# Optimization experiments

Hardware: AMD Instinct MI355X
Metric: run time of the kernel (lower is better)

Reference implementation:

```python
import jax, jax.numpy as jnp
import numpy as np

D_MODEL, D_STATE, D_CONV, EXPAND, D_EXPERT = 768, 16, 4, 2, 4
D_INNER = EXPAND * D_MODEL            # 1536
N_EXP = D_STATE // D_EXPERT           # 4 state experts
DT_RANK = -(-D_MODEL // 16)           # 48
B, L = 4, 512


def setup_inputs() -> dict:
    key = jax.random.key(0)
    ks = jax.random.split(key, 16)
    f = lambda k, shape, s=0.02: jax.random.normal(k, shape, dtype=jnp.float32) * s
    # dt bias init: inverse-softplus of dt ~ LogUniform[1e-3, 1e-1] (as in __init__)
    dt = jnp.exp(jax.random.uniform(ks[13], (D_INNER,)) * (np.log(0.1) - np.log(0.001)) + np.log(0.001))
    inv_dt = dt + jnp.log(-jnp.expm1(-dt))
    # A_log = log(arange(1..d_state)) broadcast to (d_inner, d_state)
    A_log = jnp.log(jnp.broadcast_to(jnp.arange(1, D_STATE + 1, dtype=jnp.float32), (D_INNER, D_STATE)))
    return {
        "hidden_states": jax.random.normal(ks[0], (B, L, D_MODEL), dtype=jnp.float32),
        "in_proj_w": f(ks[1], (2 * D_INNER, D_MODEL)),
        "conv_w": f(ks[2], (D_INNER, 1, D_CONV), 0.25),
        "conv_b": jnp.zeros(D_INNER, jnp.float32),
        "conv_w_b": f(ks[3], (D_INNER, 1, D_CONV), 0.25),
        "conv_b_b": jnp.zeros(D_INNER, jnp.float32),
        "x_proj_w": f(ks[4], (DT_RANK + 2 * D_STATE, D_INNER)),
        "x_proj_w_bwd": f(ks[5], (DT_RANK + 2 * D_STATE, D_INNER)),
        "dt_proj_w": f(ks[6], (D_INNER, DT_RANK), DT_RANK ** -0.5),
        "dt_proj_bias": inv_dt,
        "dt_proj_w_bwd": f(ks[7], (D_INNER, DT_RANK), DT_RANK ** -0.5),
        "dt_proj_bias_bwd": inv_dt,
        "A_log": A_log,
        "A_b_log": A_log,
        "D": jnp.ones(D_INNER, jnp.float32),
        "D_b": jnp.ones(D_INNER, jnp.float32),
        "mlp_w1": f(ks[8], (D_INNER, D_INNER)),
        "mlp_b1": jnp.zeros(D_INNER, jnp.float32),
        "mlp_w2": f(ks[9], (N_EXP, D_INNER)),
        "mlp_b2": jnp.zeros(N_EXP, jnp.float32),
        "out_proj_w": f(ks[10], (D_MODEL, D_INNER)),
    }


def _causal_conv_silu(x, w, b):
    # x: (B, D_INNER, L); depthwise causal conv, kernel D_CONV, left pad D_CONV-1
    y = jax.lax.conv_general_dilated(
        x, w, window_strides=(1,), padding=[(D_CONV - 1, 0)],
        dimension_numbers=("NCH", "OIH", "NCH"), feature_group_count=D_INNER)
    return jax.nn.silu(y + b[None, :, None])


def _selective_scan_experts(xc, Wx, Wdt, bdt, A_log):
    # xc: (B, D_INNER, L) post-conv activations. Returns per-expert outputs
    # (B, L, D_INNER, N_EXP) and xc transposed (B, L, D_INNER).
    xt = jnp.swapaxes(xc, 1, 2)                              # (B, L, D)
    x_dbl = jnp.einsum("bld,ed->ble", xt, Wx)               # (B, L, R+2N)
    dtr, Bm, Cm = jnp.split(x_dbl, [DT_RANK, DT_RANK + D_STATE], axis=-1)
    delta = jax.nn.softplus(jnp.einsum("blr,dr->bld", dtr, Wdt) + bdt)  # (B,L,D)
    A = -jnp.exp(A_log)                                      # (D, N), negative
    dA = jnp.exp(delta[..., None] * A)                       # (B,L,D,N)
    dBx = delta[..., None] * Bm[:, :, None, :] * xt[..., None]

    def step(h, inp):
        dA_t, dBx_t = inp
        h = dA_t * h + dBx_t
        return h, h

    h0 = jnp.zeros((xt.shape[0], D_INNER, D_STATE), xt.dtype)
    _, hs = jax.lax.scan(step, h0, (jnp.moveaxis(dA, 1, 0), jnp.moveaxis(dBx, 1, 0)))
    hs = jnp.moveaxis(hs, 0, 1)                              # (B,L,D,N)
    # partition d_state into N_EXP experts of D_EXPERT states; contract C per expert
    hs_e = hs.reshape(hs.shape[0], hs.shape[1], D_INNER, N_EXP, D_EXPERT)
    C_e = Cm.reshape(Cm.shape[0], Cm.shape[1], N_EXP, D_EXPERT)
    y_e = jnp.einsum("bldek,blek->blde", hs_e, C_e)          # (B,L,D,E)
    return y_e, xt


def reference(hidden_states, in_proj_w, conv_w, conv_b, conv_w_b, conv_b_b,
              x_proj_w, x_proj_w_bwd, dt_proj_w, dt_proj_bias, dt_proj_w_bwd,
              dt_proj_bias_bwd, A_log, A_b_log, D, D_b, mlp_w1, mlp_b1,
              mlp_w2, mlp_b2, out_proj_w):
    xz = jnp.einsum("bld,ed->bel", hidden_states, in_proj_w)  # (B, 2*D_INNER, L)
    x, z = jnp.split(xz, 2, axis=1)
    xb, zb = jnp.split(xz[..., ::-1], 2, axis=1)              # flipped sequence
    xc = _causal_conv_silu(x, conv_w, conv_b)
    xcb = _causal_conv_silu(xb, conv_w_b, conv_b_b)
    y_e, xt = _selective_scan_experts(xc, x_proj_w, dt_proj_w, dt_proj_bias, A_log)
    yb_e, xbt = _selective_scan_experts(xcb, x_proj_w_bwd, dt_proj_w_bwd, dt_proj_bias_bwd, A_b_log)
    # router: MLP(silu) -> sigmoid, then softmax over experts (as in torch forward)
    h1 = jax.nn.silu(jnp.einsum("bld,hd->blh", xt, mlp_w1) + mlp_b1)
    gate = jax.nn.sigmoid(jnp.einsum("blh,eh->ble", h1, mlp_w2) + mlp_b2)
    w = jax.nn.softmax(gate, axis=-1)                         # (B,L,E)
    zt, zbt = jnp.swapaxes(z, 1, 2), jnp.swapaxes(zb, 1, 2)
    # gated expert mixture + skip (D) term, then z-gate (silu), per direction.
    # Note: same forward-order router weights applied to the flipped-direction
    # outputs before the final flip, matching the torch code exactly.
    y = (jnp.einsum("blde,ble->bld", y_e, w) + xt * D) * jax.nn.silu(zt)
    yb = (jnp.einsum("blde,ble->bld", yb_e, w) + xbt * D_b) * jax.nn.silu(zbt)
    yb = yb[:, ::-1, :]                                       # flip back to forward order
    return jnp.einsum("bld,od->blo", y + yb, out_proj_w)
```

## Files before the change

### kernel.cpp

```cpp
#include <hip/hip_runtime.h>
#include <math.h>

#define ACT_NONE 0
#define ACT_SILU 1
#define ACT_SOFTPLUS 2

constexpr int kDModel = 768;
constexpr int kDInner = 1536;
constexpr int kDtRank = 48;
constexpr int kB = 4;
constexpr int kL = 512;
constexpr int kTok = kB * kL;
constexpr int kCH = 32;
constexpr int kNCH = kL / kCH;
constexpr int kSumStride = kDInner * 16;
constexpr int kXSplit = 6;
constexpr int kXKchunk = kDInner / kXSplit;

typedef __attribute__((ext_vector_type(8))) short short8v;
typedef __attribute__((ext_vector_type(8))) unsigned short ushort8v;
typedef __attribute__((ext_vector_type(4))) float f32x4;

__device__ __forceinline__ float act_apply_f(float x, int act) {
    if (act == ACT_SILU) return x / (1.f + __expf(-x));
    if (act == ACT_SOFTPLUS) return (x > 20.f) ? x : log1pf(__expf(x));
    return x;
}

__device__ __forceinline__ unsigned short f2bf(float f) {
    unsigned u = __float_as_uint(f);
    u += 0x7fff + ((u >> 16) & 1);
    return (unsigned short)(u >> 16);
}
__device__ __forceinline__ float bf2f(unsigned short h) {
    return __uint_as_float((unsigned)h << 16);
}
__device__ __forceinline__ ushort8v addbf8(ushort8v a, ushort8v b) {
    ushort8v r;
    #pragma unroll
    for (int i = 0; i < 8; ++i)
        r[i] = f2bf(bf2f(a[i]) + bf2f(b[i]));
    return r;
}

__device__ __forceinline__ void xcd_swz(int& bx, int& by, int& bz) {
    int gX = gridDim.x, gY = gridDim.y;
    int nwg = gX * gY * gridDim.z;
    int lin = bx + gX * (by + gY * bz);
    int chunk = nwg >> 3;
    int lin2 = (lin & 7) * chunk + (lin >> 3);
    bx = lin2 % gX;
    int t = lin2 / gX;
    by = t % gY;
    bz = t / gY;
}

template<int ACT, int HASBIAS, int DUAL, int SPLITK>
__global__ __launch_bounds__(256, 3)
void gemm_bf16(const unsigned short* __restrict__ A16,
               const unsigned short* __restrict__ A2,
               const unsigned short* __restrict__ W16,
               const float* __restrict__ bias,
               float* __restrict__ C,
               int M, int N, int K)
{
    __shared__ unsigned short Al[2][64][40];
    __shared__ unsigned short Bl[2][128][40];
    int bx = blockIdx.x, by = blockIdx.y, bz = blockIdx.z;
    xcd_swz(bx, by, bz);
    const int tid = threadIdx.x;
    const int row0 = by * 64;
    const int col0 = bx * 128;
    const int kc = K / SPLITK;
    const int k0base = bz * kc;

    const int srowA = tid >> 2;
    const int skA   = (tid & 3) << 3;
    const int srowB = tid >> 1;
    const int skB   = (tid & 1) << 4;

    const int w = tid >> 6;
    const int lane = tid & 63;
    const int wr = (w & 1) * 32;
    const int wc = (w >> 1) * 64;
    const int fr = lane & 15;
    const int fk = (lane >> 4) * 8;

    f32x4 acc[2][4] = {};

    const unsigned short* aptr = A16 + (size_t)(row0 + srowA) * K + k0base + skA;
    const unsigned short* aptr2 = DUAL ? (A2 + (size_t)(row0 + srowA) * K + k0base + skA) : nullptr;
    const unsigned short* bptr = W16 + (size_t)(col0 + srowB) * K + k0base + skB;

    ushort8v ra, rb0, rb1;
    auto gload = [&](int k0) {
        ra = *(const ushort8v*)(aptr + k0);
        if (DUAL) {
            ushort8v c0 = *(const ushort8v*)(aptr2 + k0);
            ra = addbf8(ra, c0);
        }
        rb0 = *(const ushort8v*)(bptr + k0);
        rb1 = *(const ushort8v*)(bptr + k0 + 8);
    };
    auto swrite = [&](int buf) {
        *(ushort8v*)&Al[buf][srowA][skA]     = ra;
        *(ushort8v*)&Bl[buf][srowB][skB]     = rb0;
        *(ushort8v*)&Bl[buf][srowB][skB + 8] = rb1;
    };

    gload(0);
    swrite(0);
    __syncthreads();

    const int nsteps = kc >> 5;
    for (int s = 0; s < nsteps; ++s) {
        const int cur = s & 1;
        if (s + 1 < nsteps) gload((s + 1) << 5);
        short8v afrag[2], bfrag[4];
        #pragma unroll
        for (int i = 0; i < 2; ++i)
            afrag[i] = *(const short8v*)&Al[cur][wr + i * 16 + fr][fk];
        #pragma unroll
        for (int j = 0; j < 4; ++j)
            bfrag[j] = *(const short8v*)&Bl[cur][wc + j * 16 + fr][fk];
        #pragma unroll
        for (int i = 0; i < 2; ++i)
            #pragma unroll
            for (int j = 0; j < 4; ++j)
                acc[i][j] = __builtin_amdgcn_mfma_f32_16x16x32_bf16(
                    afrag[i], bfrag[j], acc[i][j], 0, 0, 0);
        if (s + 1 < nsteps) swrite(cur ^ 1);
        __syncthreads();
    }

    const int orow = (lane >> 4) * 4;
    #pragma unroll
    for (int i = 0; i < 2; ++i) {
        #pragma unroll
        for (int j = 0; j < 4; ++j) {
            const int ccol = col0 + wc + j * 16 + fr;
            float bv = HASBIAS ? bias[ccol] : 0.f;
            #pragma unroll
            for (int r = 0; r < 4; ++r) {
                const int crow = row0 + wr + i * 16 + orow + r;
                float v = acc[i][j][r];
                if (SPLITK > 1) {
                    C[(size_t)bz * M * N + (size_t)crow * N + ccol] = v;
                } else {
                    v += bv;
                    C[(size_t)crow * N + ccol] = act_apply_f(v, ACT);
                }
            }
        }
    }
}

__global__ __launch_bounds__(256)
void reduce_out(const float* __restrict__ part, float* __restrict__ out, int n4)
{
    int i = blockIdx.x * 256 + threadIdx.x;
    if (i >= n4) return;
    float4 a = ((const float4*)part)[i];
    float4 b = ((const float4*)(part))[i + n4];
    float4 o;
    o.x = a.x + b.x; o.y = a.y + b.y; o.z = a.z + b.z; o.w = a.w + b.w;
    ((float4*)out)[i] = o;
}

__global__ __launch_bounds__(256, 2)
void xproj_mfma(const unsigned short* __restrict__ ahi_f, const unsigned short* __restrict__ alo_f,
                const unsigned short* __restrict__ ahi_b, const unsigned short* __restrict__ alo_b,
                const unsigned short* __restrict__ wxhi,
                const unsigned short* __restrict__ wxlo,
                float* __restrict__ xpart)
{
    __shared__ unsigned short Ah[128][40], Av[128][40], Bh[128][40], Bv[128][40];
    const int tid = threadIdx.x;
    const int row0 = blockIdx.x * 128;
    const int dir = blockIdx.y;
    const int split = blockIdx.z;
    const int ks = split * kXKchunk;

    const unsigned short* ahi = dir ? ahi_b : ahi_f;
    const unsigned short* alo = dir ? alo_b : alo_f;
    const unsigned short* whi = wxhi + (size_t)dir * 128 * kDInner;
    const unsigned short* wlo = wxlo + (size_t)dir * 128 * kDInner;

    const int srow = tid >> 1;
    const int sk   = (tid & 1) << 4;
    const int w = tid >> 6;
    const int lane = tid & 63;
    const int wr = (w >> 1) * 64;
    const int wc = (w & 1) * 64;
    const int fr = lane & 15;
    const int fk = (lane >> 4) * 8;

    f32x4 acc[4][4] = {};

    const unsigned short* pah = ahi + (size_t)(row0 + srow) * kDInner + ks + sk;
    const unsigned short* pal = alo + (size_t)(row0 + srow) * kDInner + ks + sk;
    const unsigned short* pbh = whi + (size_t)srow * kDInner + ks + sk;
    const unsigned short* pbl = wlo + (size_t)srow * kDInner + ks + sk;

    ushort8v rah0, rah1, ral0, ral1, rbh0, rbh1, rbl0, rbl1;
    auto gload = [&](int k0) {
        rah0 = *(const ushort8v*)(pah + k0); rah1 = *(const ushort8v*)(pah + k0 + 8);
        ral0 = *(const ushort8v*)(pal + k0); ral1 = *(const ushort8v*)(pal + k0 + 8);
        rbh0 = *(const ushort8v*)(pbh + k0); rbh1 = *(const ushort8v*)(pbh + k0 + 8);
        rbl0 = *(const ushort8v*)(pbl + k0); rbl1 = *(const ushort8v*)(pbl + k0 + 8);
    };
    auto swrite = [&]() {
        *(ushort8v*)&Ah[srow][sk] = rah0; *(ushort8v*)&Ah[srow][sk + 8] = rah1;
        *(ushort8v*)&Av[srow][sk] = ral0; *(ushort8v*)&Av[srow][sk + 8] = ral1;
        *(ushort8v*)&Bh[srow][sk] = rbh0; *(ushort8v*)&Bh[srow][sk + 8] = rbh1;
        *(ushort8v*)&Bv[srow][sk] = rbl0; *(ushort8v*)&Bv[srow][sk + 8] = rbl1;
    };

    gload(0);
    const int nsteps = kXKchunk >> 5;
    for (int s = 0; s < nsteps; ++s) {
        swrite();
        __syncthreads();
        if (s + 1 < nsteps) gload((s + 1) << 5);
        short8v ah[4], al[4], bh[4], bl[4];
        #pragma unroll
        for (int i = 0; i < 4; ++i) {
            ah[i] = *(const short8v*)&Ah[wr + i * 16 + fr][fk];
            al[i] = *(const short8v*)&Av[wr + i * 16 + fr][fk];
            bh[i] = *(const short8v*)&Bh[wc + i * 16 + fr][fk];
            bl[i] = *(const short8v*)&Bv[wc + i * 16 + fr][fk];
        }
        #pragma unroll
        for (int i = 0; i < 4; ++i)
            #pragma unroll
            for (int j = 0; j < 4; ++j) {
                acc[i][j] = __builtin_amdgcn_mfma_f32_16x16x32_bf16(ah[i], bh[j], acc[i][j], 0, 0, 0);
                acc[i][j] = __builtin_amdgcn_mfma_f32_16x16x32_bf16(ah[i], bl[j], acc[i][j], 0, 0, 0);
                acc[i][j] = __builtin_amdgcn_mfma_f32_16x16x32_bf16(al[i], bh[j], acc[i][j], 0, 0, 0);
            }
        __syncthreads();
    }

    float* outp = xpart + (size_t)(dir * kXSplit + split) * kTok * 80;
    const int orow = (lane >> 4) * 4;
    #pragma unroll
    for (int i = 0; i < 4; ++i)
        #pragma unroll
        for (int j = 0; j < 4; ++j) {
            const int ccol = wc + j * 16 + fr;
            if (ccol < 80) {
                #pragma unroll
                for (int r = 0; r < 4; ++r) {
                    const int crow = row0 + wr + i * 16 + orow + r;
                    outp[(size_t)crow * 80 + ccol] = acc[i][j][r];
                }
            }
        }
}

__global__ __launch_bounds__(256)
void xproj_reduce(const float* __restrict__ xpart,
                  float* __restrict__ xdbl_f, float* __restrict__ xdbl_b,
                  unsigned short* __restrict__ dtr_hi,
                  unsigned short* __restrict__ dtr_lo)
{
    int i = blockIdx.x * 256 + threadIdx.x;
    const int per = kTok * 96;
    int dir = i >= per;
    int rem = dir ? i - per : i;
    int t = rem / 96;
    int c = rem - t * 96;
    const int plane = kTok * 80;
    if (c < 80) {
        const float* base = xpart + (size_t)dir * kXSplit * plane;
        float s = 0.f;
        #pragma unroll
        for (int k = 0; k < kXSplit; ++k) s += base[(size_t)k * plane + t * 80 + c];
        (dir ? xdbl_b : xdbl_f)[(size_t)t * 80 + c] = s;
        if (c < kDtRank) {
            size_t o = ((size_t)dir * kTok + t) * 64 + c;
            unsigned short h = f2bf(s);
            dtr_hi[o] = h;
            dtr_lo[o] = f2bf(s - bf2f(h));
        }
    } else {
        int pc = c - 80 + kDtRank;
        size_t o = ((size_t)dir * kTok + t) * 64 + pc;
        dtr_hi[o] = 0;
        dtr_lo[o] = 0;
    }
}

__global__ __launch_bounds__(256, 2)
void dtproj_mfma(const unsigned short* __restrict__ dtr_hi, const unsigned short* __restrict__ dtr_lo,
                 const unsigned short* __restrict__ wdt_hi, const unsigned short* __restrict__ wdt_lo,
                 const float* __restrict__ bias_f, const float* __restrict__ bias_b,
                 float* __restrict__ delta_f, float* __restrict__ delta_b)
{
    __shared__ unsigned short Ah[128][40], Av[128][40], Bh[128][40], Bv[128][40];
    const int tid = threadIdx.x;
    const int col0 = blockIdx.x * 128;
    const int row0 = blockIdx.y * 128;
    const int dir = blockIdx.z;

    const unsigned short* ahi = dtr_hi + (size_t)dir * kTok * 64;
    const unsigned short* alo = dtr_lo + (size_t)dir * kTok * 64;
    const unsigned short* bhi = wdt_hi + (size_t)dir * kDInner * 64;
    const unsigned short* blo = wdt_lo + (size_t)dir * kDInner * 64;
    const float* bias = dir ? bias_b : bias_f;
    float* delta = dir ? delta_b : delta_f;

    const int srow = tid >> 1;
    const int sk   = (tid & 1) << 4;
    const int w = tid >> 6;
    const int lane = tid & 63;
    const int wr = (w >> 1) * 64;
    const int wc = (w & 1) * 64;
    const int fr = lane & 15;
    const int fk = (lane >> 4) * 8;

    f32x4 acc[4][4] = {};

    const unsigned short* pah = ahi + (size_t)(row0 + srow) * 64 + sk;
    const unsigned short* pal = alo + (size_t)(row0 + srow) * 64 + sk;
    const unsigned short* pbh = bhi + (size_t)(col0 + srow) * 64 + sk;
    const unsigned short* pbl = blo + (size_t)(col0 + srow) * 64 + sk;

    ushort8v rah0, rah1, ral0, ral1, rbh0, rbh1, rbl0, rbl1;
    auto gload = [&](int k0) {
        rah0 = *(const ushort8v*)(pah + k0); rah1 = *(const ushort8v*)(pah + k0 + 8);
        ral0 = *(const ushort8v*)(pal + k0); ral1 = *(const ushort8v*)(pal + k0 + 8);
        rbh0 = *(const ushort8v*)(pbh + k0); rbh1 = *(const ushort8v*)(pbh + k0 + 8);
        rbl0 = *(const ushort8v*)(pbl + k0); rbl1 = *(const ushort8v*)(pbl + k0 + 8);
    };
    auto swrite = [&]() {
        *(ushort8v*)&Ah[srow][sk] = rah0; *(ushort8v*)&Ah[srow][sk + 8] = rah1;
        *(ushort8v*)&Av[srow][sk] = ral0; *(ushort8v*)&Av[srow][sk + 8] = ral1;
        *(ushort8v*)&Bh[srow][sk] = rbh0; *(ushort8v*)&Bh[srow][sk + 8] = rbh1;
        *(ushort8v*)&Bv[srow][sk] = rbl0; *(ushort8v*)&Bv[srow][sk + 8] = rbl1;
    };

    gload(0);
    #pragma unroll
    for (int s = 0; s < 2; ++s) {
        swrite();
        __syncthreads();
        if (s == 0) gload(32);
        short8v ah[4], al[4], bh[4], bl[4];
        #pragma unroll
        for (int i = 0; i < 4; ++i) {
            ah[i] = *(const short8v*)&Ah[wr + i * 16 + fr][fk];
            al[i] = *(const short8v*)&Av[wr + i * 16 + fr][fk];
            bh[i] = *(const short8v*)&Bh[wc + i * 16 + fr][fk];
            bl[i] = *(const short8v*)&Bv[wc + i * 16 + fr][fk];
        }
        #pragma unroll
        for (int i = 0; i < 4; ++i)
            #pragma unroll
            for (int j = 0; j < 4; ++j) {
                acc[i][j] = __builtin_amdgcn_mfma_f32_16x16x32_bf16(ah[i], bh[j], acc[i][j], 0, 0, 0);
                acc[i][j] = __builtin_amdgcn_mfma_f32_16x16x32_bf16(ah[i], bl[j], acc[i][j], 0, 0, 0);
                acc[i][j] = __builtin_amdgcn_mfma_f32_16x16x32_bf16(al[i], bh[j], acc[i][j], 0, 0, 0);
            }
        __syncthreads();
    }

    const int orow = (lane >> 4) * 4;
    #pragma unroll
    for (int i = 0; i < 4; ++i)
        #pragma unroll
        for (int j = 0; j < 4; ++j) {
            const int ccol = col0 + wc + j * 16 + fr;
            const float bv = bias[ccol];
            #pragma unroll
            for (int r = 0; r < 4; ++r) {
                const int crow = row0 + wr + i * 16 + orow + r;
                float x = acc[i][j][r] + bv;
                delta[(size_t)crow * kDInner + ccol] = (x > 20.f) ? x : log1pf(__expf(x));
            }
        }
}

__global__ __launch_bounds__(256)
void convert4_kernel(const float* __restrict__ s0, unsigned short* __restrict__ d0, int n0,
                     const float* __restrict__ s1, unsigned short* __restrict__ d1, int n1,
                     const float* __restrict__ s2, unsigned short* __restrict__ d2, int n2,
                     const float* __restrict__ s3, unsigned short* __restrict__ d3, int n3)
{
    int i = blockIdx.x * 256 + threadIdx.x;
    const float* s; unsigned short* d; int loc;
    if (i < n0) { s = s0; d = d0; loc = i; }
    else if (i < n0 + n1) { s = s1; d = d1; loc = i - n0; }
    else if (i < n0 + n1 + n2) { s = s2; d = d2; loc = i - n0 - n1; }
    else if (i < n0 + n1 + n2 + n3) { s = s3; d = d3; loc = i - n0 - n1 - n2; }
    else return;
    float4 v = ((const float4*)s)[loc];
    ushort4 o;
    o.x = f2bf(v.x); o.y = f2bf(v.y); o.z = f2bf(v.z); o.w = f2bf(v.w);
    ((ushort4*)d)[loc] = o;
}

__global__ __launch_bounds__(256)
void convert_w_kernel(const float* __restrict__ Wxf, const float* __restrict__ Wxb,
                      const float* __restrict__ Wdtf, const float* __restrict__ Wdtb,
                      unsigned short* __restrict__ wxhi, unsigned short* __restrict__ wxlo,
                      unsigned short* __restrict__ wdthi, unsigned short* __restrict__ wdtlo)
{
    int i = blockIdx.x * 256 + threadIdx.x;
    const int nx = 2 * 128 * kDInner / 4;
    const int ndt_per = kDInner * 16;
    if (i < nx) {
        const int per_dir = 128 * kDInner / 4;
        int dir = i >= per_dir;
        int rem = dir ? i - per_dir : i;
        int r = rem / (kDInner / 4);
        int k4 = rem - r * (kDInner / 4);
        ushort4 oh = {0, 0, 0, 0}, ol = {0, 0, 0, 0};
        if (r < 80) {
            const float* W = dir ? Wxb : Wxf;
            float4 v = ((const float4*)W)[r * (kDInner / 4) + k4];
            oh.x = f2bf(v.x); ol.x = f2bf(v.x - bf2f(oh.x));
            oh.y = f2bf(v.y); ol.y = f2bf(v.y - bf2f(oh.y));
            oh.z = f2bf(v.z); ol.z = f2bf(v.z - bf2f(oh.z));
            oh.w = f2bf(v.w); ol.w = f2bf(v.w - bf2f(oh.w));
        }
        size_t o = ((size_t)dir * 128 + r) * kDInner + k4 * 4;
        *(ushort4*)(wxhi + o) = oh;
        *(ushort4*)(wxlo + o) = ol;
    } else {
        int j = i - nx;
        if (j >= 2 * ndt_per) return;
        int dir = j >= ndt_per;
        int rem = dir ? j - ndt_per : j;
        int r = rem >> 4;
        int k4 = rem & 15;
        ushort4 oh = {0, 0, 0, 0}, ol = {0, 0, 0, 0};
        if (k4 < 12) {
            const float* W = dir ? Wdtb : Wdtf;
            float4 v = ((const float4*)W)[r * 12 + k4];
            oh.x = f2bf(v.x); ol.x = f2bf(v.x - bf2f(oh.x));
            oh.y = f2bf(v.y); ol.y = f2bf(v.y - bf2f(oh.y));
            oh.z = f2bf(v.z); ol.z = f2bf(v.z - bf2f(oh.z));
            oh.w = f2bf(v.w); ol.w = f2bf(v.w - bf2f(oh.w));
        }
        size_t o = ((size_t)dir * kDInner + r) * 64 + k4 * 4;
        *(ushort4*)(wdthi + o) = oh;
        *(ushort4*)(wdtlo + o) = ol;
    }
}

__global__ __launch_bounds__(256)
void conv_both_kernel(const float* __restrict__ xz,
                      const float* __restrict__ w_f, const float* __restrict__ b_f,
                      const float* __restrict__ w_b, const float* __restrict__ b_b,
                      unsigned short* __restrict__ hi_f, unsigned short* __restrict__ hi_b,
                      unsigned short* __restrict__ lo_f, unsigned short* __restrict__ lo_b)
{
    __shared__ float s_x[131][64];
    const int tid = threadIdx.x;
    const int d0 = blockIdx.x * 64;
    const int b = blockIdx.y;
    const int dir = blockIdx.z;

    const float* w    = dir ? w_b : w_f;
    const float* bias = dir ? b_b : b_f;
    unsigned short* hi = dir ? hi_b : hi_f;
    unsigned short* lo = dir ? lo_b : lo_f;

    const int cd = tid & 63;
    const int lp = tid >> 6;
    float4 wv = *(const float4*)(w + (size_t)(d0 + cd) * 4);
    float bsv = bias[d0 + cd];

    for (int ch = 0; ch < 4; ++ch) {
        const int lbase = ch * 128;
        if (tid < 192) {
            int h = tid >> 6, dl = tid & 63;
            int l = lbase - 3 + h;
            float v = 0.f;
            if (l >= 0) {
                int ls = dir ? (kL - 1 - l) : l;
                v = xz[((size_t)(b * kL + ls)) * 3072 + d0 + dl];
            }
            s_x[h][dl] = v;
        }
        #pragma unroll
        for (int k = 0; k < 32; ++k) {
            int idx = k * 256 + tid;
            int li = idx >> 6, dl = idx & 63;
            int l = lbase + li;
            int ls = dir ? (kL - 1 - l) : l;
            s_x[3 + li][dl] = xz[((size_t)(b * kL + ls)) * 3072 + d0 + dl];
        }
        __syncthreads();
        #pragma unroll 4
        for (int i = 0; i < 32; ++i) {
            int li = lp * 32 + i;
            float acc = bsv;
            acc = fmaf(s_x[li + 0][cd], wv.x, acc);
            acc = fmaf(s_x[li + 1][cd], wv.y, acc);
            acc = fmaf(s_x[li + 2][cd], wv.z, acc);
            acc = fmaf(s_x[li + 3][cd], wv.w, acc);
            float o = acc / (1.f + __expf(-acc));
            size_t oi = ((size_t)(b * kL + lbase + li)) * kDInner + d0 + cd;
            unsigned short h = f2bf(o);
            hi[oi] = h;
            lo[oi] = f2bf(o - bf2f(h));
        }
        __syncthreads();
    }
}

__global__ __launch_bounds__(256)
void gate_kernel(const float* __restrict__ h1,
                 const float* __restrict__ w2,
                 const float* __restrict__ b2,
                 float* __restrict__ wgt)
{
    int wave = threadIdx.x >> 6;
    int lane = threadIdx.x & 63;
    int t = blockIdx.x * 4 + wave;
    const float* hrow = h1 + (size_t)t * kDInner;
    float acc[4] = {0.f, 0.f, 0.f, 0.f};
    for (int h = lane; h < kDInner; h += 64) {
        float hv = hrow[h];
        #pragma unroll
        for (int e = 0; e < 4; ++e)
            acc[e] = fmaf(hv, w2[e * kDInner + h], acc[e]);
    }
    #pragma unroll
    for (int e = 0; e < 4; ++e) {
        #pragma unroll
        for (int off = 32; off > 0; off >>= 1)
            acc[e] += __shfl_xor(acc[e], off);
    }
    if (lane == 0) {
        float g[4], m = -1e30f, s = 0.f;
        #pragma unroll
        for (int e = 0; e < 4; ++e) {
            g[e] = 1.f / (1.f + __expf(-(acc[e] + b2[e])));
            m = fmaxf(m, g[e]);
        }
        #pragma unroll
        for (int e = 0; e < 4; ++e) { g[e] = __expf(g[e] - m); s += g[e]; }
        float inv = 1.f / s;
        #pragma unroll
        for (int e = 0; e < 4; ++e) wgt[(size_t)t * 4 + e] = g[e] * inv;
    }
}

__global__ __launch_bounds__(256)
void scan_sum_kernel(const float* __restrict__ delta_f, const float* __restrict__ delta_b,
                     const unsigned short* __restrict__ xhi_f, const unsigned short* __restrict__ xlo_f,
                     const unsigned short* __restrict__ xhi_b, const unsigned short* __restrict__ xlo_b,
                     const float* __restrict__ xdbl_f, const float* __restrict__ xdbl_b,
                     const float* __restrict__ A_log, const float* __restrict__ A_b_log,
                     float* __restrict__ Aprod, float* __restrict__ hfin)
{
    __shared__ float s_dlt[kCH][64];
    __shared__ float s_x[kCH][64];
    __shared__ float s_b[kCH][16];

    const int tid = threadIdx.x;
    const int d0 = blockIdx.x * 64;
    const int c = blockIdx.y;
    const int z = blockIdx.z;
    const int b = z >> 1;
    const int dir = z & 1;

    const float* delta = dir ? delta_b : delta_f;
    const unsigned short* xhi = dir ? xhi_b : xhi_f;
    const unsigned short* xlo = dir ? xlo_b : xlo_f;
    const float* xdbl  = dir ? xdbl_b : xdbl_f;
    const float* Alog  = dir ? A_b_log : A_log;

    const int l0 = c * kCH;
    #pragma unroll
    for (int k = 0; k < 2; ++k) {
        int idx = k * 256 + tid;
        int l = idx >> 4, d4 = (idx & 15) << 2;
        size_t t = (size_t)(b * kL + l0 + l);
        float4 dv = *(const float4*)(delta + t * kDInner + d0 + d4);
        *(float4*)&s_dlt[l][d4] = dv;
        ushort4 hv = *(const ushort4*)(xhi + t * kDInner + d0 + d4);
        ushort4 lv = *(const ushort4*)(xlo + t * kDInner + d0 + d4);
        float4 xv;
        xv.x = bf2f(hv.x) + bf2f(lv.x); xv.y = bf2f(hv.y) + bf2f(lv.y);
        xv.z = bf2f(hv.z) + bf2f(lv.z); xv.w = bf2f(hv.w) + bf2f(lv.w);
        *(float4*)&s_x[l][d4] = xv;
    }
    if (tid < 128) {
        int l = tid >> 2, c4 = (tid & 3) << 2;
        *(float4*)&s_b[l][c4] =
            *(const float4*)(xdbl + ((size_t)(b * kL + l0 + l)) * 80 + kDtRank + c4);
    }
    const int e = tid & 3;
    const int dd = tid >> 2;
    const int d = d0 + dd;
    float An[4];
    #pragma unroll
    for (int u = 0; u < 4; ++u)
        An[u] = -__expf(Alog[(size_t)d * 16 + e * 4 + u]);
    __syncthreads();

    float h[4] = {0.f, 0.f, 0.f, 0.f};
    float sdlt = 0.f;
    const int e4 = e * 4;
    #pragma unroll 8
    for (int li = 0; li < kCH; ++li) {
        float dlt = s_dlt[li][dd];
        float xv  = s_x[li][dd];
        float dx = dlt * xv;
        sdlt += dlt;
        float4 Bv = *(const float4*)&s_b[li][e4];
        h[0] = fmaf(__expf(dlt * An[0]), h[0], dx * Bv.x);
        h[1] = fmaf(__expf(dlt * An[1]), h[1], dx * Bv.y);
        h[2] = fmaf(__expf(dlt * An[2]), h[2], dx * Bv.z);
        h[3] = fmaf(__expf(dlt * An[3]), h[3], dx * Bv.w);
    }
    size_t base = ((size_t)z * kNCH + c) * kSumStride + (size_t)d * 16 + e4;
    float4 ap, hf;
    ap.x = __expf(An[0] * sdlt); ap.y = __expf(An[1] * sdlt);
    ap.z = __expf(An[2] * sdlt); ap.w = __expf(An[3] * sdlt);
    hf.x = h[0]; hf.y = h[1]; hf.z = h[2]; hf.w = h[3];
    *(float4*)(Aprod + base) = ap;
    *(float4*)(hfin + base)  = hf;
}

__global__ __launch_bounds__(256)
void scan_comb_kernel(float* __restrict__ Aprod, const float* __restrict__ hfin)
{
    int g = blockIdx.x * 256 + threadIdx.x;
    int z = g / kSumStride;
    int rem = g - z * kSumStride;
    float h = 0.f;
    #pragma unroll
    for (int c = 0; c < kNCH; ++c) {
        size_t idx = ((size_t)z * kNCH + c) * kSumStride + rem;
        float A  = Aprod[idx];
        float hf = hfin[idx];
        Aprod[idx] = h;
        h = fmaf(A, h, hf);
    }
}

__global__ __launch_bounds__(256)
void scan_fix_kernel(const float* __restrict__ delta_f, const float* __restrict__ delta_b,
                     const unsigned short* __restrict__ xhi_f, const unsigned short* __restrict__ xlo_f,
                     const unsigned short* __restrict__ xhi_b, const unsigned short* __restrict__ xlo_b,
                     const float* __restrict__ xdbl_f, const float* __restrict__ xdbl_b,
                     const float* __restrict__ A_log, const float* __restrict__ A_b_log,
                     const float* __restrict__ Dp, const float* __restrict__ D_b,
                     const float* __restrict__ wgt, const float* __restrict__ xz,
                     const float* __restrict__ hin,
                     unsigned short* __restrict__ y16_f, unsigned short* __restrict__ y16_b)
{
    __shared__ float s_dlt[kCH][64];
    __shared__ float s_x[kCH][64];
    __shared__ float s_z[kCH][64];
    __shared__ float s_bc[kCH][32];
    __shared__ float s_w[kCH][4];

    const int tid = threadIdx.x;
    const int d0 = blockIdx.x * 64;
    const int c = blockIdx.y;
    const int z = blockIdx.z;
    const int b = z >> 1;
    const int dir = z & 1;

    const float* delta = dir ? delta_b : delta_f;
    const unsigned short* xhi = dir ? xhi_b : xhi_f;
    const unsigned short* xlo = dir ? xlo_b : xlo_f;
    const float* xdbl  = dir ? xdbl_b : xdbl_f;
    const float* Alog  = dir ? A_b_log : A_log;
    const float* Dsel  = dir ? D_b : Dp;
    unsigned short* y16 = dir ? y16_b : y16_f;

    const int l0 = c * kCH;
    #pragma unroll
    for (int k = 0; k < 2; ++k) {
        int idx = k * 256 + tid;
        int l = idx >> 4, d4 = (idx & 15) << 2;
        size_t t = (size_t)(b * kL + l0 + l);
        *(float4*)&s_dlt[l][d4] = *(const float4*)(delta + t * kDInner + d0 + d4);
        ushort4 hv = *(const ushort4*)(xhi + t * kDInner + d0 + d4);
        ushort4 lv = *(const ushort4*)(xlo + t * kDInner + d0 + d4);
        float4 xv;
        xv.x = bf2f(hv.x) + bf2f(lv.x); xv.y = bf2f(hv.y) + bf2f(lv.y);
        xv.z = bf2f(hv.z) + bf2f(lv.z); xv.w = bf2f(hv.w) + bf2f(lv.w);
        *(float4*)&s_x[l][d4] = xv;
        int lo = dir ? (kL - 1 - (l0 + l)) : (l0 + l);
        *(float4*)&s_z[l][d4] =
            *(const float4*)(xz + ((size_t)(b * kL + lo)) * 3072 + kDInner + d0 + d4);
    }
    {
        int l = tid >> 3, c4 = (tid & 7) << 2;
        *(float4*)&s_bc[l][c4] =
            *(const float4*)(xdbl + ((size_t)(b * kL + l0 + l)) * 80 + kDtRank + c4);
    }
    if (tid < 32)
        *(float4*)&s_w[tid][0] = *(const float4*)(wgt + ((size_t)(b * kL + l0 + tid)) * 4);

    const int e = tid & 3;
    const int dd = tid >> 2;
    const int d = d0 + dd;
    float An[4];
    #pragma unroll
    for (int u = 0; u < 4; ++u)
        An[u] = -__expf(Alog[(size_t)d * 16 + e * 4 + u]);
    const float Dv = Dsel[d];
    const int e4 = e * 4;
    size_t base = ((size_t)z * kNCH + c) * kSumStride + (size_t)d * 16 + e4;
    float4 h4 = *(const float4*)(hin + base);
    float h[4] = {h4.x, h4.y, h4.z, h4.w};
    __syncthreads();

    #pragma unroll 8
    for (int li = 0; li < kCH; ++li) {
        float dlt = s_dlt[li][dd];
        float xv  = s_x[li][dd];
        float dx = dlt * xv;
        float4 Bv = *(const float4*)&s_bc[li][e4];
        float4 Cv = *(const float4*)&s_bc[li][16 + e4];
        float ye = 0.f;
        h[0] = fmaf(__expf(dlt * An[0]), h[0], dx * Bv.x); ye = fmaf(h[0], Cv.x, ye);
        h[1] = fmaf(__expf(dlt * An[1]), h[1], dx * Bv.y); ye = fmaf(h[1], Cv.y, ye);
        h[2] = fmaf(__expf(dlt * An[2]), h[2], dx * Bv.z); ye = fmaf(h[2], Cv.z, ye);
        h[3] = fmaf(__expf(dlt * An[3]), h[3], dx * Bv.w); ye = fmaf(h[3], Cv.w, ye);
        float contrib = ye * s_w[li][e];
        contrib += __shfl_xor(contrib, 1);
        contrib += __shfl_xor(contrib, 2);
        if (e == 0) {
            float zv = s_z[li][dd];
            float y = (contrib + xv * Dv) * (zv / (1.f + __expf(-zv)));
            s_dlt[li][dd] = y;
        }
    }
    __syncthreads();
    #pragma unroll
    for (int k = 0; k < 2; ++k) {
        int idx = k * 256 + tid;
        int l = idx >> 4, d4 = (idx & 15) << 2;
        int lo = dir ? (kL - 1 - (l0 + l)) : (l0 + l);
        float4 yv = *(const float4*)&s_dlt[l][d4];
        ushort4 o;
        o.x = f2bf(yv.x); o.y = f2bf(yv.y); o.z = f2bf(yv.z); o.w = f2bf(yv.w);
        *(ushort4*)(y16 + ((size_t)(b * kL + lo)) * kDInner + d0 + d4) = o;
    }
}

extern "C" void kernel_launch(void* const* d_in, const int* in_sizes, int n_in,
                              void* d_out, int out_size, void* d_ws, size_t ws_size,
                              hipStream_t stream) {
    const float* hs            = (const float*)d_in[0];
    const float* in_proj_w     = (const float*)d_in[1];
    const float* conv_w        = (const float*)d_in[2];
    const float* conv_b        = (const float*)d_in[3];
    const float* conv_w_b      = (const float*)d_in[4];
    const float* conv_b_b      = (const float*)d_in[5];
    const float* x_proj_w      = (const float*)d_in[6];
    const float* x_proj_w_bwd  = (const float*)d_in[7];
    const float* dt_proj_w     = (const float*)d_in[8];
    const float* dt_proj_bias  = (const float*)d_in[9];
    const float* dt_proj_w_b   = (const float*)d_in[10];
    const float* dt_proj_bias_b= (const float*)d_in[11];
    const float* A_log         = (const float*)d_in[12];
    const float* A_b_log       = (const float*)d_in[13];
    const float* Dp            = (const float*)d_in[14];
    const float* D_b           = (const float*)d_in[15];
    const float* mlp_w1        = (const float*)d_in[16];
    const float* mlp_b1        = (const float*)d_in[17];
    const float* mlp_w2        = (const float*)d_in[18];
    const float* mlp_b2        = (const float*)d_in[19];
    const float* out_proj_w    = (const float*)d_in[20];
    float* out = (float*)d_out;

    float* ws = (float*)d_ws;
    size_t off = 0;
    auto alloc = [&](size_t n) { float* p = ws + off; off += (n + 63) & ~(size_t)63; return p; };
    float* xz      = alloc((size_t)kTok * 3072);
    unsigned short* xhi_f = (unsigned short*)alloc((size_t)kTok * kDInner / 2);
    unsigned short* xlo_f = (unsigned short*)alloc((size_t)kTok * kDInner / 2);
    unsigned short* xhi_b = (unsigned short*)alloc((size_t)kTok * kDInner / 2);
    unsigned short* xlo_b = (unsigned short*)alloc((size_t)kTok * kDInner / 2);
    float* xdbl_f  = alloc((size_t)kTok * 80);
    float* xdbl_b  = alloc((size_t)kTok * 80);
    float* delta_f = alloc((size_t)kTok * kDInner);
    float* delta_b = alloc((size_t)kTok * kDInner);
    float* h1      = alloc((size_t)kTok * kDInner);
    float* wgt     = alloc((size_t)kTok * 4);
    float* Aprod   = alloc((size_t)8 * kNCH * kSumStride);
    float* hfin    = alloc((size_t)8 * kNCH * kSumStride);
    unsigned short* hs16  = (unsigned short*)alloc((size_t)kTok * kDModel / 2);
    unsigned short* w16a  = (unsigned short*)alloc((size_t)3072 * kDModel / 2);
    unsigned short* w16b  = (unsigned short*)alloc((size_t)kDInner * kDInner / 2);
    unsigned short* w16c  = (unsigned short*)alloc((size_t)kDModel * kDInner / 2);
    unsigned short* dtr_hi  = (unsigned short*)alloc((size_t)2 * kTok * 64 / 2);
    unsigned short* dtr_lo  = (unsigned short*)alloc((size_t)2 * kTok * 64 / 2);
    unsigned short* wdt_hi  = (unsigned short*)alloc((size_t)2 * kDInner * 64 / 2);
    unsigned short* wdt_lo  = (unsigned short*)alloc((size_t)2 * kDInner * 64 / 2);

    unsigned short* wxhi = (unsigned short*)Aprod;
    unsigned short* wxlo = (unsigned short*)Aprod + 2 * 128 * kDInner;
    float* xpart = hfin;
    unsigned short* y16_f = (unsigned short*)h1;
    unsigned short* y16_b = (unsigned short*)hfin;
    float* opart = Aprod;

    dim3 blk(256);

    {
        int n0 = kTok * kDModel / 4, n1 = 3072 * kDModel / 4,
            n2 = kDInner * kDInner / 4, n3 = kDModel * kDInner / 4;
        int tot = n0 + n1 + n2 + n3;
        convert4_kernel<<<dim3((tot + 255) / 256), blk, 0, stream>>>(
            hs, hs16, n0, in_proj_w, w16a, n1, mlp_w1, w16b, n2, out_proj_w, w16c, n3);
        int totw = 2 * 128 * kDInner / 4 + 2 * kDInner * 16;
        convert_w_kernel<<<dim3((totw + 255) / 256), blk, 0, stream>>>(
            x_proj_w, x_proj_w_bwd, dt_proj_w, dt_proj_w_b, wxhi, wxlo, wdt_hi, wdt_lo);
    }

    gemm_bf16<ACT_NONE, 0, 0, 1><<<dim3(3072 / 128, kTok / 64), blk, 0, stream>>>(
        hs16, nullptr, w16a, nullptr, xz, kTok, 3072, kDModel);

    conv_both_kernel<<<dim3(kDInner / 64, kB, 2), blk, 0, stream>>>(
        xz, conv_w, conv_b, conv_w_b, conv_b_b, xhi_f, xhi_b, xlo_f, xlo_b);

    xproj_mfma<<<dim3(kTok / 128, 2, kXSplit), blk, 0, stream>>>(
        xhi_f, xlo_f, xhi_b, xlo_b, wxhi, wxlo, xpart);
    xproj_reduce<<<dim3(2 * kTok * 96 / 256), blk, 0, stream>>>(
        xpart, xdbl_f, xdbl_b, dtr_hi, dtr_lo);

    dtproj_mfma<<<dim3(kDInner / 128, kTok / 128, 2), blk, 0, stream>>>(
        dtr_hi, dtr_lo, wdt_hi, wdt_lo, dt_proj_bias, dt_proj_bias_b,
        delta_f, delta_b);

    gemm_bf16<ACT_SILU, 1, 0, 1><<<dim3(kDInner / 128, kTok / 64), blk, 0, stream>>>(
        xhi_f, nullptr, w16b, mlp_b1, h1, kTok, kDInner, kDInner);

    gate_kernel<<<dim3(kTok / 4), blk, 0, stream>>>(h1, mlp_w2, mlp_b2, wgt);

    scan_sum_kernel<<<dim3(kDInner / 64, kNCH, kB * 2), blk, 0, stream>>>(
        delta_f, delta_b, xhi_f, xlo_f, xhi_b, xlo_b, xdbl_f, xdbl_b,
        A_log, A_b_log, Aprod, hfin);
    scan_comb_kernel<<<dim3(8 * kSumStride / 256), blk, 0, stream>>>(Aprod, hfin);
    scan_fix_kernel<<<dim3(kDInner / 64, kNCH, kB * 2), blk, 0, stream>>>(
        delta_f, delta_b, xhi_f, xlo_f, xhi_b, xlo_b, xdbl_f, xdbl_b,
        A_log, A_b_log, Dp, D_b, wgt, xz, Aprod, y16_f, y16_b);

    gemm_bf16<ACT_NONE, 0, 1, 2><<<dim3(kDModel / 128, kTok / 64, 2), blk, 0, stream>>>(
        y16_f, y16_b, w16c, nullptr, opart, kTok, kDModel, kDInner);
    reduce_out<<<dim3(kTok * kDModel / 4 / 256), blk, 0, stream>>>(
        opart, out, kTok * kDModel / 4);
}
```

Baseline: 238.1 us.

## Merge conversion kernels, emit bf16 router hidden, use hardware exp2 in scan

Merges the two weight/input conversion kernels into one launch. The router MLP GEMM now writes bf16 instead of fp32, and the gate kernel reads it with vectorized 8-wide loads. The scan kernels pre-scale A by log2(e) and call v_exp_f32 directly, which drops the extra multiply inside __expf. The z-gate silu moves from a shared-memory staged load into the final output write loop. These changes cut memory traffic, launch count and ALU work, but rounding h1 to bf16 loses some precision in the gate.

After: 223.5 us. 1.07x faster.

```diff
diff --git a/kernel.cpp b/kernel.cpp
--- a/kernel.cpp
+++ b/kernel.cpp
@@ -16,6 +16,7 @@
 constexpr int kSumStride = kDInner * 16;
 constexpr int kXSplit = 6;
 constexpr int kXKchunk = kDInner / kXSplit;
+constexpr float kLog2e = 1.44269504088896340736f;
 
 typedef __attribute__((ext_vector_type(8))) short short8v;
 typedef __attribute__((ext_vector_type(8))) unsigned short ushort8v;
@@ -40,6 +41,11 @@
     #pragma unroll
     for (int i = 0; i < 8; ++i)
         r[i] = f2bf(bf2f(a[i]) + bf2f(b[i]));
+    return r;
+}
+__device__ __forceinline__ float exp2_hw(float x) {
+    float r;
+    asm("v_exp_f32 %0, %1" : "=v"(r) : "v"(x));
     return r;
 }
 
@@ -55,7 +61,7 @@
     bz = t / gY;
 }
 
-template<int ACT, int HASBIAS, int DUAL, int SPLITK>
+template<int ACT, int HASBIAS, int DUAL, int SPLITK, int OUT16 = 0>
 __global__ __launch_bounds__(256, 3)
 void gemm_bf16(const unsigned short* __restrict__ A16,
                const unsigned short* __restrict__ A2,
@@ -148,7 +154,11 @@
                     C[(size_t)bz * M * N + (size_t)crow * N + ccol] = v;
                 } else {
                     v += bv;
-                    C[(size_t)crow * N + ccol] = act_apply_f(v, ACT);
+                    v = act_apply_f(v, ACT);
+                    if (OUT16)
+                        ((unsigned short*)C)[(size_t)crow * N + ccol] = f2bf(v);
+                    else
+                        C[(size_t)crow * N + ccol] = v;
                 }
             }
         }
@@ -382,37 +392,36 @@
 }
 
 __global__ __launch_bounds__(256)
-void convert4_kernel(const float* __restrict__ s0, unsigned short* __restrict__ d0, int n0,
-                     const float* __restrict__ s1, unsigned short* __restrict__ d1, int n1,
-                     const float* __restrict__ s2, unsigned short* __restrict__ d2, int n2,
-                     const float* __restrict__ s3, unsigned short* __restrict__ d3, int n3)
+void convert_all_kernel(const float* __restrict__ s0, unsigned short* __restrict__ d0, int n0,
+                        const float* __restrict__ s1, unsigned short* __restrict__ d1, int n1,
+                        const float* __restrict__ s2, unsigned short* __restrict__ d2, int n2,
+                        const float* __restrict__ s3, unsigned short* __restrict__ d3, int n3,
+                        const float* __restrict__ Wxf, const float* __restrict__ Wxb,
+                        const float* __restrict__ Wdtf, const float* __restrict__ Wdtb,
+                        unsigned short* __restrict__ wxhi, unsigned short* __restrict__ wxlo,
+                        unsigned short* __restrict__ wdthi, unsigned short* __restrict__ wdtlo)
 {
     int i = blockIdx.x * 256 + threadIdx.x;
-    const float* s; unsigned short* d; int loc;
-    if (i < n0) { s = s0; d = d0; loc = i; }
-    else if (i < n0 + n1) { s = s1; d = d1; loc = i - n0; }
-    else if (i < n0 + n1 + n2) { s = s2; d = d2; loc = i - n0 - n1; }
-    else if (i < n0 + n1 + n2 + n3) { s = s3; d = d3; loc = i - n0 - n1 - n2; }
-    else return;
-    float4 v = ((const float4*)s)[loc];
-    ushort4 o;
-    o.x = f2bf(v.x); o.y = f2bf(v.y); o.z = f2bf(v.z); o.w = f2bf(v.w);
-    ((ushort4*)d)[loc] = o;
-}
-
-__global__ __launch_bounds__(256)
-void convert_w_kernel(const float* __restrict__ Wxf, const float* __restrict__ Wxb,
-                      const float* __restrict__ Wdtf, const float* __restrict__ Wdtb,
-                      unsigned short* __restrict__ wxhi, unsigned short* __restrict__ wxlo,
-                      unsigned short* __restrict__ wdthi, unsigned short* __restrict__ wdtlo)
-{
-    int i = blockIdx.x * 256 + threadIdx.x;
+    const int nplain = n0 + n1 + n2 + n3;
+    if (i < nplain) {
+        const float* s; unsigned short* d; int loc;
+        if (i < n0) { s = s0; d = d0; loc = i; }
+        else if (i < n0 + n1) { s = s1; d = d1; loc = i - n0; }
+        else if (i < n0 + n1 + n2) { s = s2; d = d2; loc = i - n0 - n1; }
+        else { s = s3; d = d3; loc = i - n0 - n1 - n2; }
+        float4 v = ((const float4*)s)[loc];
+        ushort4 o;
+        o.x = f2bf(v.x); o.y = f2bf(v.y); o.z = f2bf(v.z); o.w = f2bf(v.w);
+        ((ushort4*)d)[loc] = o;
+        return;
+    }
+    int j2 = i - nplain;
     const int nx = 2 * 128 * kDInner / 4;
     const int ndt_per = kDInner * 16;
-    if (i < nx) {
+    if (j2 < nx) {
         const int per_dir = 128 * kDInner / 4;
-        int dir = i >= per_dir;
-        int rem = dir ? i - per_dir : i;
+        int dir = j2 >= per_dir;
+        int rem = dir ? j2 - per_dir : j2;
         int r = rem / (kDInner / 4);
         int k4 = rem - r * (kDInner / 4);
         ushort4 oh = {0, 0, 0, 0}, ol = {0, 0, 0, 0};
@@ -428,7 +437,7 @@
         *(ushort4*)(wxhi + o) = oh;
         *(ushort4*)(wxlo + o) = ol;
     } else {
-        int j = i - nx;
+        int j = j2 - nx;
         if (j >= 2 * ndt_per) return;
         int dir = j >= ndt_per;
         int rem = dir ? j - ndt_per : j;
@@ -512,7 +521,7 @@
 }
 
 __global__ __launch_bounds__(256)
-void gate_kernel(const float* __restrict__ h1,
+void gate_kernel(const unsigned short* __restrict__ h1,
                  const float* __restrict__ w2,
                  const float* __restrict__ b2,
                  float* __restrict__ wgt)
@@ -520,13 +529,29 @@
     int wave = threadIdx.x >> 6;
     int lane = threadIdx.x & 63;
     int t = blockIdx.x * 4 + wave;
-    const float* hrow = h1 + (size_t)t * kDInner;
+    const unsigned short* hrow = h1 + (size_t)t * kDInner;
     float acc[4] = {0.f, 0.f, 0.f, 0.f};
-    for (int h = lane; h < kDInner; h += 64) {
-        float hv = hrow[h];
-        #pragma unroll
-        for (int e = 0; e < 4; ++e)
-            acc[e] = fmaf(hv, w2[e * kDInner + h], acc[e]);
+    #pragma unroll
+    for (int p = 0; p < 3; ++p) {
+        int idx = p * 512 + lane * 8;
+        ushort8v hv = *(const ushort8v*)(hrow + idx);
+        float hf[8];
+        #pragma unroll
+        for (int j = 0; j < 8; ++j) hf[j] = bf2f(hv[j]);
+        #pragma unroll
+        for (int e = 0; e < 4; ++e) {
+            const float* wp = w2 + (size_t)e * kDInner + idx;
+            float4 w0 = *(const float4*)wp;
+            float4 w1 = *(const float4*)(wp + 4);
+            acc[e] = fmaf(hf[0], w0.x, acc[e]);
+            acc[e] = fmaf(hf[1], w0.y, acc[e]);
+            acc[e] = fmaf(hf[2], w0.z, acc[e]);
+            acc[e] = fmaf(hf[3], w0.w, acc[e]);
+            acc[e] = fmaf(hf[4], w1.x, acc[e]);
+            acc[e] = fmaf(hf[5], w1.y, acc[e]);
+            acc[e] = fmaf(hf[6], w1.z, acc[e]);
+            acc[e] = fmaf(hf[7], w1.w, acc[e]);
+        }
     }
     #pragma unroll
     for (int e = 0; e < 4; ++e) {
@@ -597,10 +622,10 @@
     const int e = tid & 3;
     const int dd = tid >> 2;
     const int d = d0 + dd;
-    float An[4];
+    float An2[4];
     #pragma unroll
     for (int u = 0; u < 4; ++u)
-        An[u] = -__expf(Alog[(size_t)d * 16 + e * 4 + u]);
+        An2[u] = -__expf(Alog[(size_t)d * 16 + e * 4 + u]) * kLog2e;
     __syncthreads();
 
     float h[4] = {0.f, 0.f, 0.f, 0.f};
@@ -613,15 +638,15 @@
         float dx = dlt * xv;
         sdlt += dlt;
         float4 Bv = *(const float4*)&s_b[li][e4];
-        h[0] = fmaf(__expf(dlt * An[0]), h[0], dx * Bv.x);
-        h[1] = fmaf(__expf(dlt * An[1]), h[1], dx * Bv.y);
-        h[2] = fmaf(__expf(dlt * An[2]), h[2], dx * Bv.z);
-        h[3] = fmaf(__expf(dlt * An[3]), h[3], dx * Bv.w);
+        h[0] = fmaf(exp2_hw(dlt * An2[0]), h[0], dx * Bv.x);
+        h[1] = fmaf(exp2_hw(dlt * An2[1]), h[1], dx * Bv.y);
+        h[2] = fmaf(exp2_hw(dlt * An2[2]), h[2], dx * Bv.z);
+        h[3] = fmaf(exp2_hw(dlt * An2[3]), h[3], dx * Bv.w);
     }
     size_t base = ((size_t)z * kNCH + c) * kSumStride + (size_t)d * 16 + e4;
     float4 ap, hf;
-    ap.x = __expf(An[0] * sdlt); ap.y = __expf(An[1] * sdlt);
-    ap.z = __expf(An[2] * sdlt); ap.w = __expf(An[3] * sdlt);
+    ap.x = exp2_hw(An2[0] * sdlt); ap.y = exp2_hw(An2[1] * sdlt);
+    ap.z = exp2_hw(An2[2] * sdlt); ap.w = exp2_hw(An2[3] * sdlt);
     hf.x = h[0]; hf.y = h[1]; hf.z = h[2]; hf.w = h[3];
     *(float4*)(Aprod + base) = ap;
     *(float4*)(hfin + base)  = hf;
@@ -657,7 +682,6 @@
 {
     __shared__ float s_dlt[kCH][64];
     __shared__ float s_x[kCH][64];
-    __shared__ float s_z[kCH][64];
     __shared__ float s_bc[kCH][32];
     __shared__ float s_w[kCH][4];
 
@@ -689,9 +713,6 @@
         xv.x = bf2f(hv.x) + bf2f(lv.x); xv.y = bf2f(hv.y) + bf2f(lv.y);
         xv.z = bf2f(hv.z) + bf2f(lv.z); xv.w = bf2f(hv.w) + bf2f(lv.w);
         *(float4*)&s_x[l][d4] = xv;
-        int lo = dir ? (kL - 1 - (l0 + l)) : (l0 + l);
-        *(float4*)&s_z[l][d4] =
-            *(const float4*)(xz + ((size_t)(b * kL + lo)) * 3072 + kDInner + d0 + d4);
     }
     {
         int l = tid >> 3, c4 = (tid & 7) << 2;
@@ -704,10 +725,10 @@
     const int e = tid & 3;
     const int dd = tid >> 2;
     const int d = d0 + dd;
-    float An[4];
+    float An2[4];
     #pragma unroll
     for (int u = 0; u < 4; ++u)
-        An[u] = -__expf(Alog[(size_t)d * 16 + e * 4 + u]);
+        An2[u] = -__expf(Alog[(size_t)d * 16 + e * 4 + u]) * kLog2e;
     const float Dv = Dsel[d];
     const int e4 = e * 4;
     size_t base = ((size_t)z * kNCH + c) * kSumStride + (size_t)d * 16 + e4;
@@ -723,18 +744,15 @@
         float4 Bv = *(const float4*)&s_bc[li][e4];
         float4 Cv = *(const float4*)&s_bc[li][16 + e4];
         float ye = 0.f;
-        h[0] = fmaf(__expf(dlt * An[0]), h[0], dx * Bv.x); ye = fmaf(h[0], Cv.x, ye);
-        h[1] = fmaf(__expf(dlt * An[1]), h[1], dx * Bv.y); ye = fmaf(h[1], Cv.y, ye);
-        h[2] = fmaf(__expf(dlt * An[2]), h[2], dx * Bv.z); ye = fmaf(h[2], Cv.z, ye);
-        h[3] = fmaf(__expf(dlt * An[3]), h[3], dx * Bv.w); ye = fmaf(h[3], Cv.w, ye);
+        h[0] = fmaf(exp2_hw(dlt * An2[0]), h[0], dx * Bv.x); ye = fmaf(h[0], Cv.x, ye);
+        h[1] = fmaf(exp2_hw(dlt * An2[1]), h[1], dx * Bv.y); ye = fmaf(h[1], Cv.y, ye);
+        h[2] = fmaf(exp2_hw(dlt * An2[2]), h[2], dx * Bv.z); ye = fmaf(h[2], Cv.z, ye);
+        h[3] = fmaf(exp2_hw(dlt * An2[3]), h[3], dx * Bv.w); ye = fmaf(h[3], Cv.w, ye);
         float contrib = ye * s_w[li][e];
         contrib += __shfl_xor(contrib, 1);
         contrib += __shfl_xor(contrib, 2);
-        if (e == 0) {
-            float zv = s_z[li][dd];
-            float y = (contrib + xv * Dv) * (zv / (1.f + __expf(-zv)));
-            s_dlt[li][dd] = y;
-        }
+        if (e == 0)
+            s_dlt[li][dd] = contrib + xv * Dv;
     }
     __syncthreads();
     #pragma unroll
@@ -743,8 +761,12 @@
         int l = idx >> 4, d4 = (idx & 15) << 2;
         int lo = dir ? (kL - 1 - (l0 + l)) : (l0 + l);
         float4 yv = *(const float4*)&s_dlt[l][d4];
+        float4 zv = *(const float4*)(xz + ((size_t)(b * kL + lo)) * 3072 + kDInner + d0 + d4);
         ushort4 o;
-        o.x = f2bf(yv.x); o.y = f2bf(yv.y); o.z = f2bf(yv.z); o.w = f2bf(yv.w);
+        o.x = f2bf(yv.x * (zv.x / (1.f + __expf(-zv.x))));
+        o.y = f2bf(yv.y * (zv.y / (1.f + __expf(-zv.y))));
+        o.z = f2bf(yv.z * (zv.z / (1.f + __expf(-zv.z))));
+        o.w = f2bf(yv.w * (zv.w / (1.f + __expf(-zv.w))));
         *(ushort4*)(y16 + ((size_t)(b * kL + lo)) * kDInner + d0 + d4) = o;
     }
 }
@@ -803,6 +825,7 @@
     unsigned short* wxhi = (unsigned short*)Aprod;
     unsigned short* wxlo = (unsigned short*)Aprod + 2 * 128 * kDInner;
     float* xpart = hfin;
+    unsigned short* h1b16 = (unsigned short*)h1;
     unsigned short* y16_f = (unsigned short*)h1;
     unsigned short* y16_b = (unsigned short*)hfin;
     float* opart = Aprod;
@@ -812,12 +835,11 @@
     {
         int n0 = kTok * kDModel / 4, n1 = 3072 * kDModel / 4,
             n2 = kDInner * kDInner / 4, n3 = kDModel * kDInner / 4;
-        int tot = n0 + n1 + n2 + n3;
-        convert4_kernel<<<dim3((tot + 255) / 256), blk, 0, stream>>>(
-            hs, hs16, n0, in_proj_w, w16a, n1, mlp_w1, w16b, n2, out_proj_w, w16c, n3);
-        int totw = 2 * 128 * kDInner / 4 + 2 * kDInner * 16;
-        convert_w_kernel<<<dim3((totw + 255) / 256), blk, 0, stream>>>(
-            x_proj_w, x_proj_w_bwd, dt_proj_w, dt_proj_w_b, wxhi, wxlo, wdt_hi, wdt_lo);
+        int tot = n0 + n1 + n2 + n3 + 2 * 128 * kDInner / 4 + 2 * kDInner * 16;
+        convert_all_kernel<<<dim3((tot + 255) / 256), blk, 0, stream>>>(
+            hs, hs16, n0, in_proj_w, w16a, n1, mlp_w1, w16b, n2, out_proj_w, w16c, n3,
+            x_proj_w, x_proj_w_bwd, dt_proj_w, dt_proj_w_b,
+            wxhi, wxlo, wdt_hi, wdt_lo);
     }
 
     gemm_bf16<ACT_NONE, 0, 0, 1><<<dim3(3072 / 128, kTok / 64), blk, 0, stream>>>(
@@ -835,10 +857,10 @@
         dtr_hi, dtr_lo, wdt_hi, wdt_lo, dt_proj_bias, dt_proj_bias_b,
         delta_f, delta_b);
 
-    gemm_bf16<ACT_SILU, 1, 0, 1><<<dim3(kDInner / 128, kTok / 64), blk, 0, stream>>>(
+    gemm_bf16<ACT_SILU, 1, 0, 1, 1><<<dim3(kDInner / 128, kTok / 64), blk, 0, stream>>>(
         xhi_f, nullptr, w16b, mlp_b1, h1, kTok, kDInner, kDInner);
 
-    gate_kernel<<<dim3(kTok / 4), blk, 0, stream>>>(h1, mlp_w2, mlp_b2, wgt);
+    gate_kernel<<<dim3(kTok / 4), blk, 0, stream>>>(h1b16, mlp_w2, mlp_b2, wgt);
 
     scan_sum_kernel<<<dim3(kDInner / 64, kNCH, kB * 2), blk, 0, stream>>>(
         delta_f, delta_b, xhi_f, xlo_f, xhi_b, xlo_b, xdbl_f, xdbl_b,
```
